# Kernel tuning notes

Hardware: AMD Instinct MI355X
Metric: run time of the kernel (lower is better)

The kernel has to match this reference:

```python
import jax, jax.numpy as jnp
import numpy as np


def _laplacian_with_self_loop(adj):
    # matrix = adj + I; D^{-1/2} (sym-normalized) as in the torch code
    n = adj.shape[0]
    m = adj + jnp.eye(n, dtype=adj.dtype)
    row_sum = m.sum(axis=1)
    d_inv_sqrt = row_sum ** -0.5
    d_inv_sqrt = jnp.where(jnp.isinf(d_inv_sqrt), 0.0, d_inv_sqrt)
    # (m @ diag(d)).T @ diag(d) == (m * d[None,:]).T * d[None,:]
    return (m * d_inv_sqrt[None, :]).T * d_inv_sqrt[None, :]


MAX_DIFFUSION_STEP = 3  # K


def setup_inputs() -> dict:
    key = jax.random.key(0)
    k1, k2, k3 = jax.random.split(key, 3)
    B, N, D = 32, 512, 768
    M = MAX_DIFFUSION_STEP + 1
    inputs = jax.random.normal(k1, (B, N, D), dtype=jnp.float32)
    adj = jax.random.uniform(k2, (N, N), dtype=jnp.float32)
    # Xavier-normal-ish weights
    fan_in, fan_out = D * M, D
    std = float(np.sqrt(2.0 / (fan_in + fan_out)))
    weights = jax.random.normal(k3, (fan_in, fan_out), dtype=jnp.float32) * std
    biases = jnp.zeros((fan_out,), dtype=jnp.float32)
    return {"inputs": inputs, "adj": adj, "weights": weights, "biases": biases}


def reference(inputs, adj, weights, biases):
    B, N, D = inputs.shape
    K = MAX_DIFFUSION_STEP
    support = jax.lax.stop_gradient(_laplacian_with_self_loop(adj))  # computed under no_grad in torch

    # x0: [N, D*B]
    x0 = jnp.transpose(inputs, (1, 2, 0)).reshape(N, D * B)
    x1 = support @ x0
    xs = [x0, x1]
    for _ in range(2, K + 1):  # Chebyshev-like recurrence, small fixed K
        x2 = 2.0 * (support @ x1) - x0
        xs.append(x2)
        x1, x0 = x2, x1
    M = K + 1
    x = jnp.stack(xs, axis=0)                     # [M, N, D*B]
    x = x.reshape(M, N, D, B)
    x = jnp.transpose(x, (3, 1, 2, 0))            # [B, N, D, M]
    x = x.reshape(B * N, D * M)
    out = x @ weights + biases                    # [B*N, out]
    return out.reshape(B, N, -1)
```

## Files before the change

kernel.cpp:

```cpp
#include <hip/hip_runtime.h>

#define NN 512
#define DD 768
#define BB 32
#define KK 3072
#define NTK 96

typedef __bf16 bf16;
typedef bf16 bf16x8 __attribute__((ext_vector_type(8)));
typedef bf16 bf16x4 __attribute__((ext_vector_type(4)));
typedef float f32x4 __attribute__((ext_vector_type(4)));

typedef const unsigned int __attribute__((address_space(1)))* gas_cuintp;
typedef unsigned int __attribute__((address_space(3)))* las_uintp;

__device__ __forceinline__ void async_copy16(const void* g, void* l) {
    __builtin_amdgcn_global_load_lds((gas_cuintp)g, (las_uintp)l, 16, 0, 0);
}


__global__ void k_rowsum(const float* __restrict__ adj, float* __restrict__ dv) {
    const int i = blockIdx.x;
    const int lane = threadIdx.x;
    float s = 0.f;
#pragma unroll
    for (int j = 0; j < NN / 64; ++j) s += adj[(size_t)i * NN + lane + j * 64];
#pragma unroll
    for (int off = 32; off; off >>= 1) s += __shfl_down(s, off);
    if (lane == 0) dv[i] = rsqrtf(s + 1.0f);
}

__global__ void k_support2(const float* __restrict__ adj, const float* __restrict__ dv,
                           bf16* __restrict__ sb, bf16* __restrict__ sbt) {
    __shared__ bf16 tile[32][33];
    const int k0 = blockIdx.y * 32;
    const int n0 = blockIdx.x * 32;
    const int x = threadIdx.x;
    const int y = threadIdx.y;
    const float dn = dv[n0 + x];
#pragma unroll
    for (int q = 0; q < 4; ++q) {
        const int k = k0 + y + q * 8;
        float m = adj[(size_t)k * NN + n0 + x] + ((k == n0 + x) ? 1.0f : 0.0f);
        bf16 v = (bf16)(m * dn * dv[k]);
        sbt[(size_t)k * NN + n0 + x] = v;
        tile[y + q * 8][x] = v;
    }
    __syncthreads();
#pragma unroll
    for (int q = 0; q < 4; ++q)
        sb[(size_t)(n0 + y + q * 8) * NN + k0 + x] = tile[x][y + q * 8];
}

__global__ void k_prepwt2(const float* __restrict__ w, bf16* __restrict__ wt) {
    __shared__ bf16 tile[32][33];
    const int m = blockIdx.z;
    const int d0 = blockIdx.y * 32;
    const int o0 = blockIdx.x * 32;
    const int x = threadIdx.x, y = threadIdx.y;
#pragma unroll
    for (int q = 0; q < 4; ++q) {
        const int d = d0 + y + q * 8;
        tile[y + q * 8][x] = (bf16)w[(size_t)(d * 4 + m) * DD + o0 + x];
    }
    __syncthreads();
#pragma unroll
    for (int q = 0; q < 4; ++q)
        wt[(size_t)(o0 + y + q * 8) * KK + m * DD + d0 + x] = tile[x][y + q * 8];
}

__global__ __launch_bounds__(256) void k_prepx(const float* __restrict__ in,
                                               bf16* __restrict__ xr4,
                                               bf16* __restrict__ xt) {
    __shared__ bf16 tile[64][65];
    const int b = blockIdx.z;
    const int d0 = blockIdx.x * 64;
    const int n0 = blockIdx.y * 64;
    const int t = threadIdx.x;
    const int tx = t & 15;
    const int ty = t >> 4;
    const float* ib = in + (size_t)b * NN * DD;
#pragma unroll
    for (int q = 0; q < 4; ++q) {
        const int n = n0 + ty + q * 16;
        f32x4 v = *(const f32x4*)&ib[(size_t)n * DD + d0 + tx * 4];
        bf16x4 p;
#pragma unroll
        for (int j = 0; j < 4; ++j) p[j] = (bf16)v[j];
        *(bf16x4*)&xr4[(size_t)(b * NN + n) * KK + d0 + tx * 4] = p;
#pragma unroll
        for (int j = 0; j < 4; ++j) tile[ty + q * 16][tx * 4 + j] = p[j];
    }
    __syncthreads();
    bf16* xtb = xt + (size_t)b * DD * NN;
#pragma unroll
    for (int q = 0; q < 4; ++q) {
        const int d = ty + q * 16;
        bf16x4 p;
#pragma unroll
        for (int j = 0; j < 4; ++j) p[j] = tile[tx * 4 + j][d];
        *(bf16x4*)&xtb[(size_t)(d0 + d) * NN + n0 + tx * 4] = p;
    }
}

__device__ __forceinline__ void mfma_tile_loop(const bf16* __restrict__ A,
                                               const bf16* __restrict__ B,
                                               int lda, int ldb, int K,
                                               int i0, int j0,
                                               bf16* At, bf16* Bt, f32x4 acc[4][4]) {
    const int t = threadIdx.x;
    const int lane = t & 63;
    const int w = t >> 6;
    const int wr = w >> 1, wc = w & 1;
    const int srow = t >> 2;
    const int scol = (t & 3) * 8;
    const int fr = lane & 15;
    const int fk = (lane >> 4) * 8;
    for (int k0 = 0; k0 < K; k0 += 32) {
        __syncthreads();
        async_copy16(A + (size_t)(i0 + srow) * lda + k0 + scol, &At[t * 8]);
        async_copy16(A + (size_t)(i0 + 64 + srow) * lda + k0 + scol, &At[2048 + t * 8]);
        async_copy16(B + (size_t)(j0 + srow) * ldb + k0 + scol, &Bt[t * 8]);
        async_copy16(B + (size_t)(j0 + 64 + srow) * ldb + k0 + scol, &Bt[2048 + t * 8]);
        __syncthreads();
        bf16x8 af[4], bg[4];
#pragma unroll
        for (int mi = 0; mi < 4; ++mi)
            af[mi] = *(const bf16x8*)&At[(wr * 64 + mi * 16 + fr) * 32 + fk];
#pragma unroll
        for (int ni = 0; ni < 4; ++ni)
            bg[ni] = *(const bf16x8*)&Bt[(wc * 64 + ni * 16 + fr) * 32 + fk];
#pragma unroll
        for (int mi = 0; mi < 4; ++mi)
#pragma unroll
            for (int ni = 0; ni < 4; ++ni)
                acc[mi][ni] = __builtin_amdgcn_mfma_f32_16x16x32_bf16(
                    af[mi], bg[ni], acc[mi][ni], 0, 0, 0);
    }
}

__global__ __launch_bounds__(256) void k_poly2(const bf16* __restrict__ Sb,
                                               const bf16* __restrict__ SbT,
                                               bf16* __restrict__ P2,
                                               bf16* __restrict__ P2T) {
    __shared__ bf16 At[4096] __attribute__((aligned(16)));
    __shared__ bf16 Bt[4096] __attribute__((aligned(16)));
    const int i0 = blockIdx.y * 128, j0 = blockIdx.x * 128;
    f32x4 acc[4][4];
#pragma unroll
    for (int mi = 0; mi < 4; ++mi)
#pragma unroll
        for (int ni = 0; ni < 4; ++ni) acc[mi][ni] = f32x4{0.f, 0.f, 0.f, 0.f};
    mfma_tile_loop(Sb, SbT, NN, NN, NN, i0, j0, At, Bt, acc);
    const int t = threadIdx.x, lane = t & 63, w = t >> 6;
    const int wr = w >> 1, wc = w & 1;
    const int fr = lane & 15, rb = (lane >> 4) * 4;
#pragma unroll
    for (int mi = 0; mi < 4; ++mi)
#pragma unroll
        for (int ni = 0; ni < 4; ++ni) {
            const int ii = i0 + wr * 64 + mi * 16 + rb;
            const int jj = j0 + wc * 64 + ni * 16 + fr;
#pragma unroll
            for (int tt = 0; tt < 4; ++tt) {
                float v = 2.f * acc[mi][ni][tt] - ((ii + tt) == jj ? 1.f : 0.f);
                bf16 bv = (bf16)v;
                P2[(size_t)(ii + tt) * NN + jj] = bv;
                P2T[(size_t)jj * NN + (ii + tt)] = bv;
            }
        }
}

__global__ __launch_bounds__(256) void k_poly3(const bf16* __restrict__ Sb,
                                               const bf16* __restrict__ P2T,
                                               bf16* __restrict__ P3) {
    __shared__ bf16 At[4096] __attribute__((aligned(16)));
    __shared__ bf16 Bt[4096] __attribute__((aligned(16)));
    const int i0 = blockIdx.y * 128, j0 = blockIdx.x * 128;
    f32x4 acc[4][4];
#pragma unroll
    for (int mi = 0; mi < 4; ++mi)
#pragma unroll
        for (int ni = 0; ni < 4; ++ni) acc[mi][ni] = f32x4{0.f, 0.f, 0.f, 0.f};
    mfma_tile_loop(Sb, P2T, NN, NN, NN, i0, j0, At, Bt, acc);
    const int t = threadIdx.x, lane = t & 63, w = t >> 6;
    const int wr = w >> 1, wc = w & 1;
    const int fr = lane & 15, rb = (lane >> 4) * 4;
#pragma unroll
    for (int mi = 0; mi < 4; ++mi)
#pragma unroll
        for (int ni = 0; ni < 4; ++ni) {
            const int ii = i0 + wr * 64 + mi * 16 + rb;
            const int jj = j0 + wc * 64 + ni * 16 + fr;
#pragma unroll
            for (int tt = 0; tt < 4; ++tt) {
                float v = 2.f * acc[mi][ni][tt] - (float)Sb[(size_t)(ii + tt) * NN + jj];
                P3[(size_t)(ii + tt) * NN + jj] = (bf16)v;
            }
        }
}

__global__ __launch_bounds__(256) void k_apply(const bf16* __restrict__ P,
                                               const bf16* __restrict__ XT0,
                                               bf16* __restrict__ Xr4) {
    __shared__ bf16 At[4096] __attribute__((aligned(16)));
    __shared__ bf16 Bt[4096] __attribute__((aligned(16)));
    __shared__ bf16 epi[32 * 136] __attribute__((aligned(16)));
    const int z = blockIdx.z;
    const int m = z >> 5;
    const int b = z & 31;
    const int i0 = blockIdx.y * 128;
    const int j0 = blockIdx.x * 128;
    const bf16* A = P + (size_t)(2 * m) * NN * NN;
    const bf16* B = XT0 + (size_t)b * DD * NN;
    f32x4 acc[4][4];
#pragma unroll
    for (int mi = 0; mi < 4; ++mi)
#pragma unroll
        for (int ni = 0; ni < 4; ++ni) acc[mi][ni] = f32x4{0.f, 0.f, 0.f, 0.f};
    mfma_tile_loop(A, B, NN, NN, NN, i0, j0, At, Bt, acc);

    bf16* ob = Xr4 + (size_t)b * NN * KK + (m + 1) * DD;
    const int t = threadIdx.x, lane = t & 63, w = t >> 6;
    const int wr = w >> 1, wc = w & 1;
    const int fr = lane & 15, rb = (lane >> 4) * 4;
#pragma unroll
    for (int mi = 0; mi < 4; ++mi) {
        __syncthreads();
#pragma unroll
        for (int ni = 0; ni < 4; ++ni) {
            const int col = wc * 64 + ni * 16 + fr;
#pragma unroll
            for (int tt = 0; tt < 4; ++tt) {
                const int lr = wr * 16 + rb + tt;
                epi[lr * 136 + col] = (bf16)acc[mi][ni][tt];
            }
        }
        __syncthreads();
#pragma unroll
        for (int it = 0; it < 2; ++it) {
            const int idx = t + it * 256;
            const int lr = idx >> 4;
            const int cq = idx & 15;
            bf16x8 vv = *(const bf16x8*)&epi[lr * 136 + cq * 8];
            const int gr = i0 + (lr >> 4) * 64 + mi * 16 + (lr & 15);
            *(bf16x8*)&ob[(size_t)gr * KK + j0 + cq * 8] = vv;
        }
    }
}

__device__ __forceinline__ void stage_tile(const bf16* __restrict__ p, int rowbase,
                                           int kt, bf16* ldsdst, int t) {
    const int srow = t >> 2;
    const int sg = (t & 3) ^ ((t >> 2) & 3) ^ ((t >> 4) & 3);
    const bf16* s0 = p + (size_t)(rowbase + srow) * KK + kt * 32 + sg * 8;
    const bf16* s1 = s0 + (size_t)128 * KK;
    async_copy16(s0, ldsdst + t * 8);
    async_copy16(s1, ldsdst + 4096 + t * 8);
}

__global__ __launch_bounds__(512, 2)
void k_final512(const bf16* __restrict__ A, const bf16* __restrict__ Bw,
                const float* __restrict__ bias, float* __restrict__ out) {
    __shared__ bf16 lds[2][2][256 * 32] __attribute__((aligned(16)));
    const int t = threadIdx.x;
    const int lane = t & 63;
    const int w = t >> 6;
    const int wr = w >> 2;
    const int wc = w & 3;
    const int wgid = blockIdx.x;
    const int swz = (wgid & 7) * 24 + (wgid >> 3);
    const int i0 = (swz / 3) * 256;
    const int j0 = (swz % 3) * 256;
    const int fr = lane & 15;
    const int g = lane >> 4;
    const int rslot8 = (g ^ (fr & 3) ^ ((fr >> 2) & 3)) * 8;
    const int abase = (wr * 128 + fr) * 32 + rslot8;
    const int bbase = (wc * 64 + fr) * 32 + rslot8;

    f32x4 acc[8][4];
#pragma unroll
    for (int mi = 0; mi < 8; ++mi)
#pragma unroll
        for (int ni = 0; ni < 4; ++ni) acc[mi][ni] = f32x4{0.f, 0.f, 0.f, 0.f};

    stage_tile(A, i0, 0, &lds[0][0][0], t);
    stage_tile(Bw, j0, 0, &lds[0][1][0], t);
    stage_tile(Bw, j0, 1, &lds[1][1][0], t);
    asm volatile("s_waitcnt vmcnt(2)" ::: "memory");
    __builtin_amdgcn_s_barrier();
    __builtin_amdgcn_sched_barrier(0);

    for (int kt = 0; kt < NTK; ++kt) {
        const int cur = kt & 1;
        const bf16* As = &lds[cur][0][0];
        const bf16* Bs = &lds[cur][1][0];
        bf16x8 bg[4], af[4];
#pragma unroll
        for (int ni = 0; ni < 4; ++ni) bg[ni] = *(const bf16x8*)&Bs[bbase + ni * 512];
#pragma unroll
        for (int mi = 0; mi < 4; ++mi) af[mi] = *(const bf16x8*)&As[abase + mi * 512];
        if (kt + 1 < NTK) stage_tile(A, i0, kt + 1, &lds[cur ^ 1][0][0], t);
        __builtin_amdgcn_s_barrier();
        __builtin_amdgcn_sched_barrier(0);
        __builtin_amdgcn_s_setprio(1);
#pragma unroll
        for (int mi = 0; mi < 4; ++mi)
#pragma unroll
            for (int ni = 0; ni < 4; ++ni)
                acc[mi][ni] = __builtin_amdgcn_mfma_f32_16x16x32_bf16(
                    af[mi], bg[ni], acc[mi][ni], 0, 0, 0);
        __builtin_amdgcn_s_setprio(0);
        __builtin_amdgcn_s_barrier();
        __builtin_amdgcn_sched_barrier(0);
#pragma unroll
        for (int mi = 0; mi < 4; ++mi)
            af[mi] = *(const bf16x8*)&As[abase + 2048 + mi * 512];
        if (kt + 2 < NTK) stage_tile(Bw, j0, kt + 2, &lds[cur][1][0], t);
        __builtin_amdgcn_s_barrier();
        __builtin_amdgcn_sched_barrier(0);
        __builtin_amdgcn_s_setprio(1);
#pragma unroll
        for (int mi = 0; mi < 4; ++mi)
#pragma unroll
            for (int ni = 0; ni < 4; ++ni)
                acc[4 + mi][ni] = __builtin_amdgcn_mfma_f32_16x16x32_bf16(
                    af[mi], bg[ni], acc[4 + mi][ni], 0, 0, 0);
        __builtin_amdgcn_s_setprio(0);
        if (kt < NTK - 2) {
            asm volatile("s_waitcnt vmcnt(2)" ::: "memory");
        } else {
            asm volatile("s_waitcnt vmcnt(0)" ::: "memory");
        }
        __builtin_amdgcn_s_barrier();
        __builtin_amdgcn_sched_barrier(0);
    }

    const int rb = g * 4;
#pragma unroll
    for (int ni = 0; ni < 4; ++ni) {
        const int jj = j0 + wc * 64 + ni * 16 + fr;
        const float bv = bias[jj];
#pragma unroll
        for (int mi = 0; mi < 8; ++mi) {
            const int ii = i0 + wr * 128 + mi * 16 + rb;
#pragma unroll
            for (int tt = 0; tt < 4; ++tt)
                out[(size_t)(ii + tt) * DD + jj] = acc[mi][ni][tt] + bv;
        }
    }
}

extern "C" void kernel_launch(void* const* d_in, const int* in_sizes, int n_in,
                              void* d_out, int out_size, void* d_ws, size_t ws_size,
                              hipStream_t stream) {
    const float* inputs = (const float*)d_in[0];
    const float* adj = (const float*)d_in[1];
    const float* weights = (const float*)d_in[2];
    const float* biases = (const float*)d_in[3];
    float* out = (float*)d_out;

    char* ws = (char*)d_ws;
    const size_t SQ = (size_t)NN * NN * 2;
    float* dv = (float*)(ws + 0);
    bf16* Sb = (bf16*)(ws + 4096);
    bf16* SbT = (bf16*)(ws + 4096 + SQ);
    bf16* P2 = (bf16*)(ws + 4096 + 2 * SQ);
    bf16* P2T = (bf16*)(ws + 4096 + 3 * SQ);
    bf16* P3 = (bf16*)(ws + 4096 + 4 * SQ);
    bf16* WtK = (bf16*)(ws + 4096 + 5 * SQ);
    char* p = ws + 4096 + 5 * SQ + (size_t)DD * KK * 2;
    bf16* XT0 = (bf16*)p;
    bf16* Xr4 = (bf16*)(p + (size_t)BB * NN * DD * 2);

    k_rowsum<<<NN, 64, 0, stream>>>(adj, dv);
    k_support2<<<dim3(16, 16), dim3(32, 8), 0, stream>>>(adj, dv, Sb, SbT);
    k_prepwt2<<<dim3(24, 24, 4), dim3(32, 8), 0, stream>>>(weights, WtK);
    k_prepx<<<dim3(DD / 64, NN / 64, BB), 256, 0, stream>>>(inputs, Xr4, XT0);

    k_poly2<<<dim3(4, 4), 256, 0, stream>>>(Sb, SbT, P2, P2T);
    k_poly3<<<dim3(4, 4), 256, 0, stream>>>(Sb, P2T, P3);

    k_apply<<<dim3(DD / 128, NN / 128, 3 * BB), 256, 0, stream>>>(Sb, XT0, Xr4);

    k_final512<<<192, 512, 0, stream>>>(Xr4, WtK, biases, out);
}
```

Baseline: 302.0 us.

## Unify apply and final GEMMs into templated 128x384 triple-buffered MFMA kernel

Replaces the separate k_apply (128x128 tiles, 256 threads, one polynomial per launch slice) and k_final512 (256x256 tiles, double buffer) with a single templated k_mm kernel using 128x384 tiles and a 3-stage async LDS pipeline. The diffusion step is recast as XT0 times a concatenated [S;P2;P3] matrix, so all three polynomial applications are one GEMM with a transposed scatter epilogue into Xr4. The final GEMM now uses 256 workgroups instead of 192, which is meant to improve CU occupancy and latency hiding. The trade-offs are more LDS per block and a different register footprint.

```diff
diff --git a/kernel.cpp b/kernel.cpp
--- a/kernel.cpp
+++ b/kernel.cpp
@@ -4,7 +4,6 @@
 #define DD 768
 #define BB 32
 #define KK 3072
-#define NTK 96
 
 typedef __bf16 bf16;
 typedef bf16 bf16x8 __attribute__((ext_vector_type(8)));
@@ -200,153 +199,122 @@
         }
 }
 
-__global__ __launch_bounds__(256) void k_apply(const bf16* __restrict__ P,
-                                               const bf16* __restrict__ XT0,
-                                               bf16* __restrict__ Xr4) {
-    __shared__ bf16 At[4096] __attribute__((aligned(16)));
-    __shared__ bf16 Bt[4096] __attribute__((aligned(16)));
-    __shared__ bf16 epi[32 * 136] __attribute__((aligned(16)));
-    const int z = blockIdx.z;
-    const int m = z >> 5;
-    const int b = z & 31;
-    const int i0 = blockIdx.y * 128;
-    const int j0 = blockIdx.x * 128;
-    const bf16* A = P + (size_t)(2 * m) * NN * NN;
-    const bf16* B = XT0 + (size_t)b * DD * NN;
-    f32x4 acc[4][4];
-#pragma unroll
-    for (int mi = 0; mi < 4; ++mi)
-#pragma unroll
-        for (int ni = 0; ni < 4; ++ni) acc[mi][ni] = f32x4{0.f, 0.f, 0.f, 0.f};
-    mfma_tile_loop(A, B, NN, NN, NN, i0, j0, At, Bt, acc);
-
-    bf16* ob = Xr4 + (size_t)b * NN * KK + (m + 1) * DD;
-    const int t = threadIdx.x, lane = t & 63, w = t >> 6;
-    const int wr = w >> 1, wc = w & 1;
-    const int fr = lane & 15, rb = (lane >> 4) * 4;
-#pragma unroll
-    for (int mi = 0; mi < 4; ++mi) {
-        __syncthreads();
-#pragma unroll
-        for (int ni = 0; ni < 4; ++ni) {
-            const int col = wc * 64 + ni * 16 + fr;
-#pragma unroll
-            for (int tt = 0; tt < 4; ++tt) {
-                const int lr = wr * 16 + rb + tt;
-                epi[lr * 136 + col] = (bf16)acc[mi][ni][tt];
-            }
-        }
-        __syncthreads();
-#pragma unroll
-        for (int it = 0; it < 2; ++it) {
-            const int idx = t + it * 256;
-            const int lr = idx >> 4;
-            const int cq = idx & 15;
-            bf16x8 vv = *(const bf16x8*)&epi[lr * 136 + cq * 8];
-            const int gr = i0 + (lr >> 4) * 64 + mi * 16 + (lr & 15);
-            *(bf16x8*)&ob[(size_t)gr * KK + j0 + cq * 8] = vv;
-        }
-    }
-}
-
-__device__ __forceinline__ void stage_tile(const bf16* __restrict__ p, int rowbase,
-                                           int kt, bf16* ldsdst, int t) {
-    const int srow = t >> 2;
-    const int sg = (t & 3) ^ ((t >> 2) & 3) ^ ((t >> 4) & 3);
-    const bf16* s0 = p + (size_t)(rowbase + srow) * KK + kt * 32 + sg * 8;
-    const bf16* s1 = s0 + (size_t)128 * KK;
-    async_copy16(s0, ldsdst + t * 8);
-    async_copy16(s1, ldsdst + 4096 + t * 8);
-}
-
-__global__ __launch_bounds__(512, 2)
-void k_final512(const bf16* __restrict__ A, const bf16* __restrict__ Bw,
-                const float* __restrict__ bias, float* __restrict__ out) {
-    __shared__ bf16 lds[2][2][256 * 32] __attribute__((aligned(16)));
+template <int NT, int LDA, int LDB, int NWG, int NJ, int EPI>
+__global__ __launch_bounds__(512) void k_mm(const bf16* __restrict__ A,
+                                            const bf16* __restrict__ B,
+                                            const float* __restrict__ bias,
+                                            float* __restrict__ outF,
+                                            bf16* __restrict__ outS) {
+    __shared__ bf16 lds[3 * 4096 + 3 * 12288] __attribute__((aligned(16)));
+    bf16* ldsA = lds;
+    bf16* ldsB = lds + 3 * 4096;
     const int t = threadIdx.x;
     const int lane = t & 63;
     const int w = t >> 6;
     const int wr = w >> 2;
     const int wc = w & 3;
-    const int wgid = blockIdx.x;
-    const int swz = (wgid & 7) * 24 + (wgid >> 3);
-    const int i0 = (swz / 3) * 256;
-    const int j0 = (swz % 3) * 256;
+    const int wg = blockIdx.x;
+    const int swz = (wg & 7) * (NWG / 8) + (wg >> 3);
+    const int itile = swz / NJ;
+    const int jtile = swz % NJ;
+    const int i0 = itile * 128;
+    const int j0 = jtile * 384;
     const int fr = lane & 15;
     const int g = lane >> 4;
     const int rslot8 = (g ^ (fr & 3) ^ ((fr >> 2) & 3)) * 8;
-    const int abase = (wr * 128 + fr) * 32 + rslot8;
-    const int bbase = (wc * 64 + fr) * 32 + rslot8;
-
-    f32x4 acc[8][4];
-#pragma unroll
-    for (int mi = 0; mi < 8; ++mi)
-#pragma unroll
-        for (int ni = 0; ni < 4; ++ni) acc[mi][ni] = f32x4{0.f, 0.f, 0.f, 0.f};
-
-    stage_tile(A, i0, 0, &lds[0][0][0], t);
-    stage_tile(Bw, j0, 0, &lds[0][1][0], t);
-    stage_tile(Bw, j0, 1, &lds[1][1][0], t);
-    asm volatile("s_waitcnt vmcnt(2)" ::: "memory");
+    const int abase = (wr * 64 + fr) * 32 + rslot8;
+    const int bbase = (wc * 96 + fr) * 32 + rslot8;
+    const int srow = t >> 2;
+    const int sg8 = ((t & 3) ^ ((t >> 2) & 3) ^ ((t >> 4) & 3)) * 8;
+
+    f32x4 acc[4][6];
+#pragma unroll
+    for (int mi = 0; mi < 4; ++mi)
+#pragma unroll
+        for (int ni = 0; ni < 6; ++ni) acc[mi][ni] = f32x4{0.f, 0.f, 0.f, 0.f};
+
+    auto stage = [&](int kt) {
+        const int buf = kt % 3;
+        async_copy16(A + (size_t)(i0 + srow) * LDA + kt * 32 + sg8,
+                     ldsA + buf * 4096 + t * 8);
+        const bf16* bs = B + (size_t)(j0 + srow) * LDB + kt * 32 + sg8;
+#pragma unroll
+        for (int q = 0; q < 3; ++q)
+            async_copy16(bs + (size_t)(128 * q) * LDB,
+                         ldsB + buf * 12288 + q * 4096 + t * 8);
+    };
+
+    stage(0);
+    stage(1);
+    asm volatile("s_waitcnt vmcnt(4)" ::: "memory");
     __builtin_amdgcn_s_barrier();
     __builtin_amdgcn_sched_barrier(0);
 
-    for (int kt = 0; kt < NTK; ++kt) {
-        const int cur = kt & 1;
-        const bf16* As = &lds[cur][0][0];
-        const bf16* Bs = &lds[cur][1][0];
-        bf16x8 bg[4], af[4];
-#pragma unroll
-        for (int ni = 0; ni < 4; ++ni) bg[ni] = *(const bf16x8*)&Bs[bbase + ni * 512];
+    for (int kt = 0; kt < NT; ++kt) {
+        const int buf = kt % 3;
+        if (kt + 2 < NT) stage(kt + 2);
+        const bf16* As = ldsA + buf * 4096;
+        const bf16* Bs = ldsB + buf * 12288;
+        bf16x8 af[4], bg[6];
 #pragma unroll
         for (int mi = 0; mi < 4; ++mi) af[mi] = *(const bf16x8*)&As[abase + mi * 512];
-        if (kt + 1 < NTK) stage_tile(A, i0, kt + 1, &lds[cur ^ 1][0][0], t);
-        __builtin_amdgcn_s_barrier();
-        __builtin_amdgcn_sched_barrier(0);
+#pragma unroll
+        for (int ni = 0; ni < 6; ++ni) bg[ni] = *(const bf16x8*)&Bs[bbase + ni * 512];
         __builtin_amdgcn_s_setprio(1);
 #pragma unroll
         for (int mi = 0; mi < 4; ++mi)
 #pragma unroll
-            for (int ni = 0; ni < 4; ++ni)
+            for (int ni = 0; ni < 6; ++ni)
                 acc[mi][ni] = __builtin_amdgcn_mfma_f32_16x16x32_bf16(
                     af[mi], bg[ni], acc[mi][ni], 0, 0, 0);
         __builtin_amdgcn_s_setprio(0);
+        if (kt + 2 < NT) {
+            asm volatile("s_waitcnt vmcnt(4)" ::: "memory");
+        } else {
+            asm volatile("s_waitcnt vmcnt(0)" ::: "memory");
+        }
         __builtin_amdgcn_s_barrier();
         __builtin_amdgcn_sched_barrier(0);
-#pragma unroll
-        for (int mi = 0; mi < 4; ++mi)
-            af[mi] = *(const bf16x8*)&As[abase + 2048 + mi * 512];
-        if (kt + 2 < NTK) stage_tile(Bw, j0, kt + 2, &lds[cur][1][0], t);
-        __builtin_amdgcn_s_barrier();
-        __builtin_amdgcn_sched_barrier(0);
-        __builtin_amdgcn_s_setprio(1);
-#pragma unroll
-        for (int mi = 0; mi < 4; ++mi)
-#pragma unroll
-            for (int ni = 0; ni < 4; ++ni)
-                acc[4 + mi][ni] = __builtin_amdgcn_mfma_f32_16x16x32_bf16(
-                    af[mi], bg[ni], acc[4 + mi][ni], 0, 0, 0);
-        __builtin_amdgcn_s_setprio(0);
-        if (kt < NTK - 2) {
-            asm volatile("s_waitcnt vmcnt(2)" ::: "memory");
-        } else {
-            asm volatile("s_waitcnt vmcnt(0)" ::: "memory");
-        }
-        __builtin_amdgcn_s_barrier();
-        __builtin_amdgcn_sched_barrier(0);
     }
 
     const int rb = g * 4;
-#pragma unroll
-    for (int ni = 0; ni < 4; ++ni) {
-        const int jj = j0 + wc * 64 + ni * 16 + fr;
-        const float bv = bias[jj];
-#pragma unroll
-        for (int mi = 0; mi < 8; ++mi) {
-            const int ii = i0 + wr * 128 + mi * 16 + rb;
-#pragma unroll
-            for (int tt = 0; tt < 4; ++tt)
-                out[(size_t)(ii + tt) * DD + jj] = acc[mi][ni][tt] + bv;
+    if constexpr (EPI == 0) {
+#pragma unroll
+        for (int ni = 0; ni < 6; ++ni) {
+            const int jj = j0 + wc * 96 + ni * 16 + fr;
+            const float bv = bias[jj];
+#pragma unroll
+            for (int mi = 0; mi < 4; ++mi) {
+                const int ii = i0 + wr * 64 + mi * 16 + rb;
+#pragma unroll
+                for (int tt = 0; tt < 4; ++tt)
+                    outF[(size_t)(ii + tt) * DD + jj] = acc[mi][ni][tt] + bv;
+            }
+        }
+    } else {
+        const int bblk = itile / 6;
+        const int d0 = (itile % 6) * 128;
+        bf16* epi = lds;
+#pragma unroll
+        for (int ni = 0; ni < 6; ++ni) {
+            __builtin_amdgcn_s_barrier();
+#pragma unroll
+            for (int mi = 0; mi < 4; ++mi) {
+                bf16x4 p;
+#pragma unroll
+                for (int tt = 0; tt < 4; ++tt) p[tt] = (bf16)acc[mi][ni][tt];
+                *(bf16x4*)&epi[(wc * 16 + fr) * 136 + wr * 64 + mi * 16 + rb] = p;
+            }
+            __builtin_amdgcn_s_barrier();
+            const int row_e = t >> 3;
+            const int cpos = (t & 7) * 16;
+            const int mnl = (row_e >> 4) * 96 + ni * 16 + (row_e & 15);
+            const int mn = jtile * 384 + mnl;
+            const int m = mn >> 9;
+            const int n = mn & 511;
+            bf16* dst = outS + ((size_t)(bblk * 512 + n)) * KK + (m + 1) * DD + d0 + cpos;
+            *(bf16x8*)dst = *(const bf16x8*)&epi[row_e * 136 + cpos];
+            *(bf16x8*)(dst + 8) = *(const bf16x8*)&epi[row_e * 136 + cpos + 8];
         }
     }
 }
@@ -363,16 +331,18 @@
     char* ws = (char*)d_ws;
     const size_t SQ = (size_t)NN * NN * 2;
     float* dv = (float*)(ws + 0);
-    bf16* Sb = (bf16*)(ws + 4096);
-    bf16* SbT = (bf16*)(ws + 4096 + SQ);
-    bf16* P2 = (bf16*)(ws + 4096 + 2 * SQ);
-    bf16* P2T = (bf16*)(ws + 4096 + 3 * SQ);
-    bf16* P3 = (bf16*)(ws + 4096 + 4 * SQ);
+    bf16* Pcat = (bf16*)(ws + 4096);
+    bf16* SbT = (bf16*)(ws + 4096 + 3 * SQ);
+    bf16* P2T = (bf16*)(ws + 4096 + 4 * SQ);
     bf16* WtK = (bf16*)(ws + 4096 + 5 * SQ);
     char* p = ws + 4096 + 5 * SQ + (size_t)DD * KK * 2;
     bf16* XT0 = (bf16*)p;
     bf16* Xr4 = (bf16*)(p + (size_t)BB * NN * DD * 2);
 
+    bf16* Sb = Pcat;
+    bf16* P2 = Pcat + (size_t)NN * NN;
+    bf16* P3 = Pcat + (size_t)2 * NN * NN;
+
     k_rowsum<<<NN, 64, 0, stream>>>(adj, dv);
     k_support2<<<dim3(16, 16), dim3(32, 8), 0, stream>>>(adj, dv, Sb, SbT);
     k_prepwt2<<<dim3(24, 24, 4), dim3(32, 8), 0, stream>>>(weights, WtK);
@@ -381,7 +351,9 @@
     k_poly2<<<dim3(4, 4), 256, 0, stream>>>(Sb, SbT, P2, P2T);
     k_poly3<<<dim3(4, 4), 256, 0, stream>>>(Sb, P2T, P3);
 
-    k_apply<<<dim3(DD / 128, NN / 128, 3 * BB), 256, 0, stream>>>(Sb, XT0, Xr4);
-
-    k_final512<<<192, 512, 0, stream>>>(Xr4, WtK, biases, out);
-}
+    k_mm<16, 512, 512, 768, 4, 1><<<768, 512, 0, stream>>>(
+        XT0, Pcat, nullptr, nullptr, Xr4);
+
+    k_mm<96, KK, KK, 256, 2, 0><<<256, 512, 0, stream>>>(
+        Xr4, WtK, biases, out, nullptr);
+}
```

Result: faster. 283.8 us (-6.0%).
